# Kernel tuning notes

Measured on AMD Instinct MI355X. Metric: run time of the kernel, lower is better.

## Reference

```python
import jax, jax.numpy as jnp
import numpy as np

N = 1024          # num_nodes
E = 16384         # num_edges (avg degree 16)
D = 256           # in_channels
P = 2.0           # PairwiseDistance p
SELF_ADD = 0.5
UPPER_BOUND = 2.0
# scores lie in [SELF_ADD, 1+SELF_ADD] = [0.5, 1.5], so the greedy loop adds
# at most ceil(UPPER_BOUND / 0.5) = 4 edges; 6 masked steps is a safe bound.
MAX_STEPS = 6


def setup_inputs() -> dict:
    key = jax.random.key(0)
    k1, k2 = jax.random.split(key)
    x = jax.random.normal(k1, (N, D), dtype=jnp.float32)
    edge_index = jax.random.randint(k2, (2, E), 0, N, dtype=jnp.int64)
    return {"x": x, "edge_index": edge_index}


def _edge_scores(x, src, dst):
    # compute_distance_score: L2 pairwise distance, min-max normalized, + self_add
    diff = x[src] - x[dst]                      # [E, D]
    dist = jnp.sqrt(jnp.sum(diff * diff, axis=-1))
    dist = (dist - dist.min()) / (dist.max() - dist.min())
    return dist + SELF_ADD                      # [E]


def _search_all(edge_score, src, dst):
    # Vectorized version of node__cluster_search: for each seed node i, greedily
    # add the min-score edge leaving the cluster until total score >= UPPER_BOUND
    # or no frontier edge exists. Fixed-length masked scan == original while-loop.
    def search(i):
        inc = jnp.zeros((N,), bool).at[i].set(True)      # in_cluster mask
        row = jnp.zeros((N,), jnp.float32)               # node_score_matrix row
        tot = jnp.float32(0.0)

        def step(state, _):
            inc, row, tot = state
            valid = inc[src] & ~inc[dst]                 # frontier edges [E]
            active = (tot < UPPER_BOUND) & jnp.any(valid)
            masked = jnp.where(valid, edge_score, jnp.inf)
            e = jnp.argmin(masked)                       # min-score frontier edge
            s = edge_score[e]
            u, v = src[e], dst[e]
            inc2 = inc.at[v].set(True)
            row2 = row.at[u].add(s * 0.5).at[v].add(s * 0.5)
            inc = jnp.where(active, inc2, inc)
            row = jnp.where(active, row2, row)
            tot = jnp.where(active, tot + s, tot)
            return (inc, row, tot), None

        (inc, row, tot), _ = jax.lax.scan(step, (inc, row, tot), None, length=MAX_STEPS)
        return inc.astype(jnp.float32), row

    return jax.vmap(search)(jnp.arange(N))


def _keep_first_unique_rows(assign):
    # np.unique(..., axis=0) dedup, shape-static variant: keep first occurrence of
    # each distinct binary row, zero out duplicates. Double random-hash row compare.
    rng = np.random.default_rng(12345)
    r1 = jnp.asarray(rng.integers(1, 2**20, size=(N,)), dtype=jnp.int32)
    r2 = jnp.asarray(rng.integers(1, 2**20, size=(N,)), dtype=jnp.int32)
    ai = assign.astype(jnp.int32)
    h1, h2 = ai @ r1, ai @ r2
    eq = (h1[:, None] == h1[None, :]) & (h2[:, None] == h2[None, :])  # [N, N]
    dup = jnp.any(jnp.tril(eq, k=-1), axis=1)
    return (~dup).astype(jnp.float32)


def reference(x, edge_index):
    src, dst = edge_index[0], edge_index[1]
    edge_score = _edge_scores(x, src, dst)
    assign, nsm = _search_all(edge_score, src, dst)      # [N, N], [N, N]

    keep = _keep_first_unique_rows(assign)               # [N]
    assign_k = assign * keep[:, None]
    nsm_k = nsm * keep[:, None]

    # dense adjacency (to_dense_adj), pooled adjacency, binarize, drop self-loops
    adj = jnp.zeros((N, N), jnp.float32).at[src, dst].add(1.0)
    adj_new = assign_k @ adj @ assign_k.T
    adj_new = (adj_new > 0).astype(jnp.float32) * (1.0 - jnp.eye(N, dtype=jnp.float32))

    x_new = nsm_k @ x                                    # pooled features [N, D]
    return adj_new, x_new, assign_k, nsm_k
```

## Files before the change

### kernel.cpp

```cpp
#include <hip/hip_runtime.h>
#include <cstdint>

#define NN 1024
#define NE 16384
#define DF 256
#define UB 2.0f
#define MAXSEL 6
#define CAP 128
#define NB (NE/4)
#define DSTR 16

typedef unsigned long long u64;

__global__ void k_zero(uint4* __restrict__ p) {
    p[blockIdx.x * 256 + threadIdx.x] = make_uint4(0, 0, 0, 0);
}

__global__ void k_dist_build(const float* __restrict__ x, const int* __restrict__ src,
                             const int* __restrict__ dst, int* __restrict__ deg,
                             u64* __restrict__ slots,
                             uint32_t* __restrict__ pmin, uint32_t* __restrict__ pmax) {
    __shared__ uint32_t smin[4], smax[4];
    int wid = threadIdx.x >> 6;
    int lane = threadIdx.x & 63;
    int e = blockIdx.x * 4 + wid;
    int u = src[e], v = dst[e];
    float4 a = ((const float4*)(x + (size_t)u * DF))[lane];
    float4 b = ((const float4*)(x + (size_t)v * DF))[lane];
    float d0 = a.x - b.x, d1 = a.y - b.y, d2 = a.z - b.z, d3 = a.w - b.w;
    double s = (double)d0 * d0 + (double)d1 * d1 + (double)d2 * d2 + (double)d3 * d3;
    for (int off = 32; off; off >>= 1) s += __shfl_xor(s, off, 64);
    if (lane == 0) {
        float dist = sqrtf((float)s);
        uint32_t db = __float_as_uint(dist);
        int pos = atomicAdd(&deg[u * DSTR], 1);
        if (pos < CAP)
            slots[(size_t)u * CAP + pos] =
                ((u64)db << 24) | ((u64)(uint32_t)e << 10) | (u64)(uint32_t)v;
        smin[wid] = db;
        smax[wid] = db;
    }
    __syncthreads();
    if (threadIdx.x == 0) {
        pmin[blockIdx.x] = min(min(smin[0], smin[1]), min(smin[2], smin[3]));
        pmax[blockIdx.x] = max(max(smax[0], smax[1]), max(smax[2], smax[3]));
    }
}

__global__ void k_search(const int* __restrict__ deg, const u64* __restrict__ slots,
                         const uint32_t* __restrict__ pmin, const uint32_t* __restrict__ pmax,
                         const int* __restrict__ src,
                         uint32_t* __restrict__ masks, uint32_t* __restrict__ maskT,
                         int* __restrict__ selU, int* __restrict__ selV,
                         float* __restrict__ selS, int* __restrict__ selCnt,
                         u64* __restrict__ sig) {
    __shared__ uint32_t inc[32];
    __shared__ int members[8];
    __shared__ float s_tot;
    __shared__ int s_nmem;
    int i = blockIdx.x, lane = threadIdx.x;
    if (lane < 32) inc[lane] = 0;

    uint32_t mnb = 0xFFFFFFFFu, mxb = 0u;
    const uint4* p4n = (const uint4*)pmin;
    const uint4* p4x = (const uint4*)pmax;
    for (int k = lane; k < NB / 4; k += 64) {
        uint4 a = p4n[k], b = p4x[k];
        mnb = min(mnb, min(min(a.x, a.y), min(a.z, a.w)));
        mxb = max(mxb, max(max(b.x, b.y), max(b.z, b.w)));
    }
    for (int off = 32; off; off >>= 1) {
        uint32_t oa = (uint32_t)__shfl_xor((int)mnb, off, 64);
        uint32_t ob = (uint32_t)__shfl_xor((int)mxb, off, 64);
        mnb = min(mnb, oa);
        mxb = max(mxb, ob);
    }
    float MN = __uint_as_float(mnb);
    float MX = __uint_as_float(mxb);

    if (lane == 0) {
        inc[i >> 5] = 1u << (i & 31);
        members[0] = i;
        s_tot = 0.0f;
        s_nmem = 1;
    }
    __syncthreads();
    int cnt = 0;
    for (int step = 0; step < MAXSEL; ++step) {
        if (s_tot >= UB) break;
        u64 best = ~0ull;
        int nm = s_nmem;
        for (int m = 0; m < nm; ++m) {
            int u = members[m];
            int dc = min(deg[u * DSTR], CAP);
            const u64* sl = slots + (size_t)u * CAP;
            for (int k = lane; k < dc; k += 64) {
                u64 t = sl[k];
                int v = (int)(t & 1023);
                if (!((inc[v >> 5] >> (v & 31)) & 1u) && t < best) best = t;
            }
        }
        for (int off = 32; off; off >>= 1) {
            u64 o = __shfl_xor(best, off, 64);
            if (o < best) best = o;
        }
        if (best == ~0ull) break;
        if (lane == 0) {
            uint32_t db = (uint32_t)(best >> 24);
            int e = (int)((best >> 10) & 0x3FFF);
            int v = (int)(best & 1023);
            float dd = __uint_as_float(db);
            float s = (dd - MN) / (MX - MN) + 0.5f;
            int u = src[e];
            inc[v >> 5] |= 1u << (v & 31);
            members[s_nmem++] = v;
            selU[i * 8 + cnt] = u;
            selV[i * 8 + cnt] = v;
            selS[i * 8 + cnt] = s;
            s_tot += s;
        }
        cnt++;
        __syncthreads();
    }
    __syncthreads();
    if (lane == 0) {
        selCnt[i] = cnt;
        u64 h = 1469598103934665603ull;
        for (int w = 0; w < 32; ++w) { h ^= inc[w]; h *= 1099511628211ull; }
        sig[i] = h;
    }
    if (lane < 32) masks[(size_t)i * 32 + lane] = inc[lane];
    if (lane < s_nmem) {
        int n = members[lane];
        atomicOr(&maskT[(size_t)n * 32 + (i >> 5)], 1u << (i & 31));
    }
}

__global__ void k_rows(const float* __restrict__ x, const int* __restrict__ deg,
                       const u64* __restrict__ slots,
                       const uint32_t* __restrict__ masks, const uint32_t* __restrict__ maskT,
                       const u64* __restrict__ sig,
                       const int* __restrict__ selU, const int* __restrict__ selV,
                       const float* __restrict__ selS, const int* __restrict__ selCnt,
                       float* __restrict__ outAdj, float* __restrict__ outAs,
                       float* __restrict__ outNsm, float* __restrict__ outX) {
    __shared__ u64 sigL[NN];
    __shared__ uint32_t keepb[32];
    __shared__ uint32_t R[32], MI[32], orow[32];
    __shared__ uint32_t part[8][32];
    __shared__ int su[8], ssv[8];
    __shared__ float ss[8];
    __shared__ int s_c;
    int i = blockIdx.x, t = threadIdx.x;

    for (int j = t; j < NN; j += 256) sigL[j] = sig[j];
    if (t < 32) { keepb[t] = 0; R[t] = 0; MI[t] = masks[(size_t)i * 32 + t]; }
    if (t == 0) s_c = selCnt[i];
    if (t < 8) { su[t] = selU[i*8+t]; ssv[t] = selV[i*8+t]; ss[t] = selS[i*8+t]; }
    __syncthreads();

    for (int q = 0; q < 4; ++q) {
        int j = t + q * 256;
        int cj = selCnt[j];
        u64 sj = sigL[j];
        bool dup = false;
        for (int k = 0; k < cj && !dup; ++k) {
            int v = selV[j * 8 + k];
            if (v < j && sigL[v] == sj) dup = true;
        }
        if (!dup) atomicOr(&keepb[j >> 5], 1u << (j & 31));
    }

    int c = s_c;
    for (int m = 0; m <= c; ++m) {
        int u = (m == 0) ? i : ssv[m - 1];
        int dc = min(deg[u * DSTR], CAP);
        const u64* sl = slots + (size_t)u * CAP;
        for (int k = t; k < dc; k += 256) {
            int v = (int)(sl[k] & 1023);
            atomicOr(&R[v >> 5], 1u << (v & 31));
        }
    }
    __syncthreads();
    int kp = (keepb[i >> 5] >> (i & 31)) & 1;

    int g = t >> 5, l = t & 31;
    uint32_t acc = 0;
    if (kp) {
        for (int wi = g; wi < 32; wi += 8) {
            uint32_t bits = R[wi];
            while (bits) {
                int b = __ffs(bits) - 1;
                bits &= bits - 1;
                acc |= maskT[((size_t)(wi * 32 + b)) * 32 + l];
            }
        }
    }
    part[g][l] = acc;
    __syncthreads();
    if (t < 32) {
        uint32_t o = 0;
        for (int gg = 0; gg < 8; ++gg) o |= part[gg][t];
        orow[t] = o & keepb[t];
    }
    __syncthreads();

    int j0 = t * 4;
    int w = j0 >> 5, sh = j0 & 31;
    float4 vadj = {0,0,0,0}, vas = {0,0,0,0}, vnsm = {0,0,0,0};
    if (kp) {
        uint32_t ob = orow[w] >> sh;
        uint32_t mb = MI[w] >> sh;
        vadj.x = ((ob     ) & 1) && (j0     != i) ? 1.0f : 0.0f;
        vadj.y = ((ob >> 1) & 1) && (j0 + 1 != i) ? 1.0f : 0.0f;
        vadj.z = ((ob >> 2) & 1) && (j0 + 2 != i) ? 1.0f : 0.0f;
        vadj.w = ((ob >> 3) & 1) && (j0 + 3 != i) ? 1.0f : 0.0f;
        vas.x = (mb      & 1) ? 1.0f : 0.0f;
        vas.y = ((mb>>1) & 1) ? 1.0f : 0.0f;
        vas.z = ((mb>>2) & 1) ? 1.0f : 0.0f;
        vas.w = ((mb>>3) & 1) ? 1.0f : 0.0f;
        for (int k = 0; k < c; ++k) {
            float h = ss[k] * 0.5f;
            int u = su[k], v = ssv[k];
            vnsm.x += ((u == j0    ) ? h : 0.0f) + ((v == j0    ) ? h : 0.0f);
            vnsm.y += ((u == j0 + 1) ? h : 0.0f) + ((v == j0 + 1) ? h : 0.0f);
            vnsm.z += ((u == j0 + 2) ? h : 0.0f) + ((v == j0 + 2) ? h : 0.0f);
            vnsm.w += ((u == j0 + 3) ? h : 0.0f) + ((v == j0 + 3) ? h : 0.0f);
        }
    }
    ((float4*)outAdj)[(size_t)i * (NN/4) + t] = vadj;
    ((float4*)outAs )[(size_t)i * (NN/4) + t] = vas;
    ((float4*)outNsm)[(size_t)i * (NN/4) + t] = vnsm;

    float accx = 0.0f;
    if (kp) {
        for (int k = 0; k < c; ++k) {
            float h = ss[k] * 0.5f;
            accx += h * x[(size_t)su[k] * DF + t];
            accx += h * x[(size_t)ssv[k] * DF + t];
        }
    }
    outX[(size_t)i * DF + t] = accx;
}

extern "C" void kernel_launch(void* const* d_in, const int* in_sizes, int n_in,
                              void* d_out, int out_size, void* d_ws, size_t ws_size,
                              hipStream_t stream) {
    const float* x = (const float*)d_in[0];
    const int* ei = (const int*)d_in[1];
    const int* src = ei;
    const int* dst = ei + NE;

    float* out = (float*)d_out;
    float* out_adj = out;
    float* out_x   = out + (size_t)NN * NN;
    float* out_as  = out_x + (size_t)NN * DF;
    float* out_nsm = out_as + (size_t)NN * NN;

    char* w = (char*)d_ws;
    u64*      slots = (u64*)w;       w += (size_t)NN * CAP * 8;
    u64*      sig   = (u64*)w;       w += (size_t)NN * 8;
    int*      deg   = (int*)w;       w += (size_t)NN * DSTR * 4;
    uint32_t* maskT = (uint32_t*)w;  w += (size_t)NN * 32 * 4;
    uint32_t* pmin  = (uint32_t*)w;  w += (size_t)NB * 4;
    uint32_t* pmax  = (uint32_t*)w;  w += (size_t)NB * 4;
    uint32_t* masks = (uint32_t*)w;  w += (size_t)NN * 32 * 4;
    int*      selU  = (int*)w;       w += (size_t)NN * 8 * 4;
    int*      selV  = (int*)w;       w += (size_t)NN * 8 * 4;
    float*    selS  = (float*)w;     w += (size_t)NN * 8 * 4;
    int*      selCnt= (int*)w;       w += (size_t)NN * 4;

    k_zero<<<48, 256, 0, stream>>>((uint4*)deg);
    k_dist_build<<<NB, 256, 0, stream>>>(x, src, dst, deg, slots, pmin, pmax);
    k_search<<<NN, 64, 0, stream>>>(deg, slots, pmin, pmax, src,
                                    masks, maskT, selU, selV, selS, selCnt, sig);
    k_rows<<<NN, 256, 0, stream>>>(x, deg, slots, masks, maskT, sig,
                                   selU, selV, selS, selCnt,
                                   out_adj, out_as, out_nsm, out_x);
}
```

Measured before the change: 41.59 us.

## Process 16 edges per block, flatten frontier scan, pack duplicate candidates

The distance kernel now uses 16 lanes per edge, so each block handles 16 edges and min/max is reduced with shuffles, giving 1024 blocks instead of 4096. The search kernel builds prefix offsets over member degrees and scans all member frontier slots in one flat loop, which should improve lane utilisation. It also packs member ids smaller than the seed into a 64-bit word so the duplicate check in the row kernel reads one value. The maskT gather loop is manually unrolled by two. These add extra syncs per step and a short serial prefix sum.

```diff
diff --git a/kernel.cpp b/kernel.cpp
--- a/kernel.cpp
+++ b/kernel.cpp
@@ -7,7 +7,7 @@
 #define UB 2.0f
 #define MAXSEL 6
 #define CAP 128
-#define NB (NE/4)
+#define NB2 1024
 #define DSTR 16
 
 typedef unsigned long long u64;
@@ -21,27 +21,49 @@
                              u64* __restrict__ slots,
                              uint32_t* __restrict__ pmin, uint32_t* __restrict__ pmax) {
     __shared__ uint32_t smin[4], smax[4];
-    int wid = threadIdx.x >> 6;
-    int lane = threadIdx.x & 63;
-    int e = blockIdx.x * 4 + wid;
+    int t = threadIdx.x;
+    int wid = t >> 6, lane = t & 63;
+    int c16 = lane & 15;
+    int e = blockIdx.x * 16 + wid * 4 + (lane >> 4);
     int u = src[e], v = dst[e];
-    float4 a = ((const float4*)(x + (size_t)u * DF))[lane];
-    float4 b = ((const float4*)(x + (size_t)v * DF))[lane];
-    float d0 = a.x - b.x, d1 = a.y - b.y, d2 = a.z - b.z, d3 = a.w - b.w;
-    double s = (double)d0 * d0 + (double)d1 * d1 + (double)d2 * d2 + (double)d3 * d3;
-    for (int off = 32; off; off >>= 1) s += __shfl_xor(s, off, 64);
-    if (lane == 0) {
-        float dist = sqrtf((float)s);
-        uint32_t db = __float_as_uint(dist);
+    const float4* xa = (const float4*)(x + (size_t)u * DF);
+    const float4* xb = (const float4*)(x + (size_t)v * DF);
+    float4 a0 = xa[c16],      b0 = xb[c16];
+    float4 a1 = xa[c16 + 16], b1 = xb[c16 + 16];
+    float4 a2 = xa[c16 + 32], b2 = xb[c16 + 32];
+    float4 a3 = xa[c16 + 48], b3 = xb[c16 + 48];
+    double s = 0.0;
+    {
+        float d;
+        d = a0.x-b0.x; s += (double)d*d;  d = a0.y-b0.y; s += (double)d*d;
+        d = a0.z-b0.z; s += (double)d*d;  d = a0.w-b0.w; s += (double)d*d;
+        d = a1.x-b1.x; s += (double)d*d;  d = a1.y-b1.y; s += (double)d*d;
+        d = a1.z-b1.z; s += (double)d*d;  d = a1.w-b1.w; s += (double)d*d;
+        d = a2.x-b2.x; s += (double)d*d;  d = a2.y-b2.y; s += (double)d*d;
+        d = a2.z-b2.z; s += (double)d*d;  d = a2.w-b2.w; s += (double)d*d;
+        d = a3.x-b3.x; s += (double)d*d;  d = a3.y-b3.y; s += (double)d*d;
+        d = a3.z-b3.z; s += (double)d*d;  d = a3.w-b3.w; s += (double)d*d;
+    }
+    s += __shfl_xor(s, 1, 64);
+    s += __shfl_xor(s, 2, 64);
+    s += __shfl_xor(s, 4, 64);
+    s += __shfl_xor(s, 8, 64);
+    uint32_t db = __float_as_uint(sqrtf((float)s));
+    if (c16 == 0) {
         int pos = atomicAdd(&deg[u * DSTR], 1);
         if (pos < CAP)
             slots[(size_t)u * CAP + pos] =
                 ((u64)db << 24) | ((u64)(uint32_t)e << 10) | (u64)(uint32_t)v;
-        smin[wid] = db;
-        smax[wid] = db;
-    }
-    __syncthreads();
-    if (threadIdx.x == 0) {
+    }
+    uint32_t mnv = db, mxv = db;
+    uint32_t o;
+    o = (uint32_t)__shfl_xor((int)mnv, 16, 64); mnv = min(mnv, o);
+    o = (uint32_t)__shfl_xor((int)mnv, 32, 64); mnv = min(mnv, o);
+    o = (uint32_t)__shfl_xor((int)mxv, 16, 64); mxv = max(mxv, o);
+    o = (uint32_t)__shfl_xor((int)mxv, 32, 64); mxv = max(mxv, o);
+    if (lane == 0) { smin[wid] = mnv; smax[wid] = mxv; }
+    __syncthreads();
+    if (t == 0) {
         pmin[blockIdx.x] = min(min(smin[0], smin[1]), min(smin[2], smin[3]));
         pmax[blockIdx.x] = max(max(smax[0], smax[1]), max(smax[2], smax[3]));
     }
@@ -53,9 +75,10 @@
                          uint32_t* __restrict__ masks, uint32_t* __restrict__ maskT,
                          int* __restrict__ selU, int* __restrict__ selV,
                          float* __restrict__ selS, int* __restrict__ selCnt,
-                         u64* __restrict__ sig) {
+                         u64* __restrict__ sig, u64* __restrict__ dc64) {
     __shared__ uint32_t inc[32];
     __shared__ int members[8];
+    __shared__ int degL[8], offL[9];
     __shared__ float s_tot;
     __shared__ int s_nmem;
     int i = blockIdx.x, lane = threadIdx.x;
@@ -64,7 +87,7 @@
     uint32_t mnb = 0xFFFFFFFFu, mxb = 0u;
     const uint4* p4n = (const uint4*)pmin;
     const uint4* p4x = (const uint4*)pmax;
-    for (int k = lane; k < NB / 4; k += 64) {
+    for (int k = lane; k < NB2 / 4; k += 64) {
         uint4 a = p4n[k], b = p4x[k];
         mnb = min(mnb, min(min(a.x, a.y), min(a.z, a.w)));
         mxb = max(mxb, max(max(b.x, b.y), max(b.z, b.w)));
@@ -88,17 +111,22 @@
     int cnt = 0;
     for (int step = 0; step < MAXSEL; ++step) {
         if (s_tot >= UB) break;
+        int nm = s_nmem;
+        if (lane < nm) degL[lane] = min(deg[members[lane] * DSTR], CAP);
+        __syncthreads();
+        if (lane == 0) {
+            offL[0] = 0;
+            for (int m = 0; m < nm; ++m) offL[m + 1] = offL[m] + degL[m];
+        }
+        __syncthreads();
+        int T = offL[nm];
         u64 best = ~0ull;
-        int nm = s_nmem;
-        for (int m = 0; m < nm; ++m) {
-            int u = members[m];
-            int dc = min(deg[u * DSTR], CAP);
-            const u64* sl = slots + (size_t)u * CAP;
-            for (int k = lane; k < dc; k += 64) {
-                u64 t = sl[k];
-                int v = (int)(t & 1023);
-                if (!((inc[v >> 5] >> (v & 31)) & 1u) && t < best) best = t;
-            }
+        for (int f = lane; f < T; f += 64) {
+            int m = 0;
+            while (f >= offL[m + 1]) ++m;
+            u64 en = slots[(size_t)members[m] * CAP + (f - offL[m])];
+            int v = (int)(en & 1023);
+            if (!((inc[v >> 5] >> (v & 31)) & 1u) && en < best) best = en;
         }
         for (int off = 32; off; off >>= 1) {
             u64 o = __shfl_xor(best, off, 64);
@@ -128,6 +156,12 @@
         u64 h = 1469598103934665603ull;
         for (int w = 0; w < 32; ++w) { h ^= inc[w]; h *= 1099511628211ull; }
         sig[i] = h;
+        u64 d = 0; int nc = 0;
+        for (int k = 1; k < s_nmem; ++k) {
+            int v = members[k];
+            if (v < i) { d |= ((u64)(uint32_t)v) << (4 + 10 * nc); ++nc; }
+        }
+        dc64[i] = d | (u64)nc;
     }
     if (lane < 32) masks[(size_t)i * 32 + lane] = inc[lane];
     if (lane < s_nmem) {
@@ -139,7 +173,7 @@
 __global__ void k_rows(const float* __restrict__ x, const int* __restrict__ deg,
                        const u64* __restrict__ slots,
                        const uint32_t* __restrict__ masks, const uint32_t* __restrict__ maskT,
-                       const u64* __restrict__ sig,
+                       const u64* __restrict__ sig, const u64* __restrict__ dc64,
                        const int* __restrict__ selU, const int* __restrict__ selV,
                        const float* __restrict__ selS, const int* __restrict__ selCnt,
                        float* __restrict__ outAdj, float* __restrict__ outAs,
@@ -161,12 +195,13 @@
 
     for (int q = 0; q < 4; ++q) {
         int j = t + q * 256;
-        int cj = selCnt[j];
+        u64 d = dc64[j];
+        int cj = (int)(d & 15);
         u64 sj = sigL[j];
         bool dup = false;
-        for (int k = 0; k < cj && !dup; ++k) {
-            int v = selV[j * 8 + k];
-            if (v < j && sigL[v] == sj) dup = true;
+        for (int k = 0; k < cj; ++k) {
+            int v = (int)((d >> (4 + 10 * k)) & 1023);
+            if (sigL[v] == sj) { dup = true; break; }
         }
         if (!dup) atomicOr(&keepb[j >> 5], 1u << (j & 31));
     }
@@ -190,9 +225,13 @@
         for (int wi = g; wi < 32; wi += 8) {
             uint32_t bits = R[wi];
             while (bits) {
-                int b = __ffs(bits) - 1;
-                bits &= bits - 1;
-                acc |= maskT[((size_t)(wi * 32 + b)) * 32 + l];
+                int b0 = __ffs(bits) - 1; bits &= bits - 1;
+                uint32_t v0 = maskT[((size_t)(wi * 32 + b0)) * 32 + l];
+                if (bits) {
+                    int b1 = __ffs(bits) - 1; bits &= bits - 1;
+                    v0 |= maskT[((size_t)(wi * 32 + b1)) * 32 + l];
+                }
+                acc |= v0;
             }
         }
     }
@@ -260,10 +299,11 @@
     char* w = (char*)d_ws;
     u64*      slots = (u64*)w;       w += (size_t)NN * CAP * 8;
     u64*      sig   = (u64*)w;       w += (size_t)NN * 8;
+    u64*      dc64  = (u64*)w;       w += (size_t)NN * 8;
     int*      deg   = (int*)w;       w += (size_t)NN * DSTR * 4;
     uint32_t* maskT = (uint32_t*)w;  w += (size_t)NN * 32 * 4;
-    uint32_t* pmin  = (uint32_t*)w;  w += (size_t)NB * 4;
-    uint32_t* pmax  = (uint32_t*)w;  w += (size_t)NB * 4;
+    uint32_t* pmin  = (uint32_t*)w;  w += (size_t)NB2 * 4;
+    uint32_t* pmax  = (uint32_t*)w;  w += (size_t)NB2 * 4;
     uint32_t* masks = (uint32_t*)w;  w += (size_t)NN * 32 * 4;
     int*      selU  = (int*)w;       w += (size_t)NN * 8 * 4;
     int*      selV  = (int*)w;       w += (size_t)NN * 8 * 4;
@@ -271,10 +311,10 @@
     int*      selCnt= (int*)w;       w += (size_t)NN * 4;
 
     k_zero<<<48, 256, 0, stream>>>((uint4*)deg);
-    k_dist_build<<<NB, 256, 0, stream>>>(x, src, dst, deg, slots, pmin, pmax);
+    k_dist_build<<<NB2, 256, 0, stream>>>(x, src, dst, deg, slots, pmin, pmax);
     k_search<<<NN, 64, 0, stream>>>(deg, slots, pmin, pmax, src,
-                                    masks, maskT, selU, selV, selS, selCnt, sig);
-    k_rows<<<NN, 256, 0, stream>>>(x, deg, slots, masks, maskT, sig,
+                                    masks, maskT, selU, selV, selS, selCnt, sig, dc64);
+    k_rows<<<NN, 256, 0, stream>>>(x, deg, slots, masks, maskT, sig, dc64,
                                    selU, selV, selS, selCnt,
                                    out_adj, out_as, out_nsm, out_x);
 }
```

Result: faster. 34.86 us (median of 5 runs) (-16.2%).
